# Kernel tuning notes

Measured on AMD Instinct MI355X. Metric: run time of the kernel, lower is better.

Reference implementation:

```python
import jax, jax.numpy as jnp
import numpy as np

NUM_RELATION = 500
NUM_ENTITY = 100000
EMBED_DIM = 64
B, N = 8192, 128
MASK_BIG = 1e19


def setup_inputs() -> dict:
    key = jax.random.key(0)
    k1, k2, k3, k4, k5, k6, k7, k8 = jax.random.split(key, 8)
    inp = {
        "input": jax.random.normal(k1, (B, N, EMBED_DIM), dtype=jnp.float32),
        "neighbor": jax.random.randint(k2, (B, N, 2), 0, NUM_ENTITY + 1, dtype=jnp.int64),
        "query_relation_id": jax.random.randint(k3, (B,), 0, 2 * NUM_RELATION, dtype=jnp.int64),
        "weight": jax.random.uniform(k4, (B, N, 2), dtype=jnp.float32),
        # learned parameters (xavier-normal-like init)
        "mlp_w_weight": jax.random.normal(k5, (NUM_ENTITY * 2 + 1, EMBED_DIM), dtype=jnp.float32) * 0.02,
        "qrel_weight": jax.random.normal(k6, (NUM_RELATION * 2, EMBED_DIM), dtype=jnp.float32) * 0.02,
        "att_w": jax.random.normal(k7, (EMBED_DIM * 2, EMBED_DIM * 2), dtype=jnp.float32) * 0.05,
        "att_v": jax.random.normal(k8, (1, EMBED_DIM * 2), dtype=jnp.float32) * 0.05,
    }
    return inp


def reference(input, neighbor, query_relation_id, weight, mlp_w_weight, qrel_weight, att_w, att_v):
    # neighbor channels: relation id (indexes mlp_w), entity id (indexes mask tables)
    input_relation = neighbor[:, :, 0]
    input_entity = neighbor[:, :, 1]

    r = mlp_w_weight[input_relation]                         # [B,N,D] gather
    # hyperplane transform: e - <e, r_hat> r_hat  (F.normalize with eps=1e-12)
    norm = jnp.maximum(jnp.linalg.norm(r, axis=2, keepdims=True), 1e-12)
    normed = r / norm
    transformed = input - jnp.sum(input * normed, axis=2, keepdims=True) * normed

    # mask_emb: 1 for real entities, 0 for padding entity (id == NUM_ENTITY)
    mask = (input_entity < NUM_ENTITY).astype(transformed.dtype)[:, :, None]
    transformed = transformed * mask

    query = qrel_weight[query_relation_id][:, None, :]       # [B,1,D]
    query = jnp.broadcast_to(query, (query.shape[0], transformed.shape[1], query.shape[2]))

    # MLP attention: tanh([q; t] W) . v
    hidden = jnp.tanh(jnp.concatenate([query, transformed], axis=2) @ att_w)  # [B,N,2D]
    attention_logit = jnp.sum(hidden * att_v[0], axis=2)      # [B,N]

    # mask_weight: subtract 1e19 at padding entities
    mask_logit = jnp.where(input_entity == NUM_ENTITY, jnp.float32(MASK_BIG), jnp.float32(0.0))
    attention_logit = attention_logit - mask_logit

    attention_weight = jax.nn.softmax(attention_logit, axis=1)
    attention_weight = attention_weight + weight[:, :, 0] / (weight[:, :, 1] + 1)

    output = jnp.sum(transformed * attention_weight[:, :, None], axis=1)  # [B,D]
    return output, attention_weight
```

## Files before the change

### kernel.cpp

```cpp
#include <hip/hip_runtime.h>
#include <hip/hip_bf16.h>

#define NB 8192
#define NE 100000

typedef __bf16 bf16x8 __attribute__((ext_vector_type(8)));
typedef __bf16 bf16x4 __attribute__((ext_vector_type(4)));
typedef float  f32x4  __attribute__((ext_vector_type(4)));

template<int C>
__device__ __forceinline__ float dpp_mov(float v) {
  return __int_as_float(__builtin_amdgcn_update_dpp(
      0, __float_as_int(v), C, 0xF, 0xF, true));
}

__device__ __forceinline__ float red16(float v) {
  v += dpp_mov<0xB1>(v);
  v += dpp_mov<0x4E>(v);
  v += dpp_mov<0x141>(v);
  v += dpp_mov<0x140>(v);
  return v;
}

__device__ __forceinline__ float fast_tanh(float x) {
  float e = __expf(-2.0f * fabsf(x));
  float t = (1.0f - e) * __builtin_amdgcn_rcpf(1.0f + e);
  return copysignf(t, x);
}

__global__ void prep_kernel(const float* __restrict__ att_w,
                            const float* __restrict__ qrel,
                            __bf16* __restrict__ wsf,
                            float*  __restrict__ qpart) {
  const int t = threadIdx.x;
  const int bid = blockIdx.x;
  if (bid == 0) {
    for (int i = t; i < 8192; i += 128) {
      int e  = i & 7;
      int l  = (i >> 3) & 63;
      int ks = (i >> 9) & 1;
      int tc = i >> 10;
      int k = ks * 32 + ((l >> 4) << 3) + e;
      int j = tc * 16 + (l & 15);
      wsf[i] = (__bf16)att_w[(64 + k) * 128 + j];
    }
  } else {
    int rid = bid - 1;
    float acc = 0.f;
    for (int k = 0; k < 64; ++k)
      acc += qrel[rid * 64 + k] * att_w[k * 128 + t];
    qpart[rid * 128 + t] = acc;
  }
}

__global__ __launch_bounds__(256, 6)
void attn_kernel(const float* __restrict__ inp,
                 const int*   __restrict__ nb,
                 const int*   __restrict__ qid_p,
                 const float* __restrict__ wgt,
                 const float* __restrict__ mlp,
                 const float* __restrict__ attv,
                 const __bf16* __restrict__ wsf,
                 const float* __restrict__ qpart_t,
                 float* __restrict__ out) {
  __shared__ __attribute__((aligned(16))) __bf16 T16[128][72];
  __shared__ float qp[128], plog[128], awl[128], wrat[128];
  __shared__ float part[4][64];

  const int t    = threadIdx.x;
  const int lane = t & 63;
  const int w    = t >> 6;
  const int g    = lane >> 4;
  const int q    = lane & 15;
  const int b    = blockIdx.x;

  if (t < 128) {
    int qid = qid_p[b];
    qp[t] = qpart_t[qid * 128 + t];
    float2 w01 = reinterpret_cast<const float2*>(wgt)[(size_t)b * 128 + t];
    wrat[t] = w01.x / (w01.y + 1.0f);
  }

  {
    int2 re[8];
#pragma unroll
    for (int i = 0; i < 8; ++i) {
      int n = w * 32 + i * 4 + g;
      re[i] = *reinterpret_cast<const int2*>(&nb[((size_t)b * 128 + n) * 2]);
    }
#pragma unroll
    for (int i = 0; i < 8; ++i) {
      int n = w * 32 + i * 4 + g;
      f32x4 iv = *reinterpret_cast<const f32x4*>(&inp[((size_t)b * 128 + n) * 64 + q * 4]);
      f32x4 rv = *reinterpret_cast<const f32x4*>(&mlp[(size_t)re[i].x * 64 + q * 4]);
      float s1 = red16(rv[0]*rv[0] + rv[1]*rv[1] + rv[2]*rv[2] + rv[3]*rv[3]);
      float s2 = red16(iv[0]*rv[0] + iv[1]*rv[1] + iv[2]*rv[2] + iv[3]*rv[3]);
      float f  = s2 / fmaxf(s1, 1e-24f);
      float m  = (re[i].y >= NE) ? 0.0f : 1.0f;
      bf16x4 tv;
#pragma unroll
      for (int j = 0; j < 4; ++j) tv[j] = (__bf16)((iv[j] - f * rv[j]) * m);
      *reinterpret_cast<bf16x4*>(&T16[n][q * 4]) = tv;
    }
  }
  __syncthreads();

  float vv[8];
#pragma unroll
  for (int tc = 0; tc < 8; ++tc) vv[tc] = attv[tc * 16 + q];

  f32x4 acc[2][8];
#pragma unroll
  for (int tc = 0; tc < 8; ++tc) {
    float qv = qp[tc * 16 + q];
    acc[0][tc] = f32x4{qv, qv, qv, qv};
    acc[1][tc] = f32x4{qv, qv, qv, qv};
  }
  bf16x8 af[2][2];
#pragma unroll
  for (int tr = 0; tr < 2; ++tr) {
    int row = w * 32 + tr * 16 + q;
    af[tr][0] = *reinterpret_cast<const bf16x8*>(&T16[row][g * 8]);
    af[tr][1] = *reinterpret_cast<const bf16x8*>(&T16[row][g * 8 + 32]);
  }
#pragma unroll
  for (int tc = 0; tc < 8; ++tc) {
    bf16x8 b0 = *reinterpret_cast<const bf16x8*>(wsf + ((tc * 2 + 0) * 64 + lane) * 8);
    bf16x8 b1 = *reinterpret_cast<const bf16x8*>(wsf + ((tc * 2 + 1) * 64 + lane) * 8);
    acc[0][tc] = __builtin_amdgcn_mfma_f32_16x16x32_bf16(af[0][0], b0, acc[0][tc], 0, 0, 0);
    acc[1][tc] = __builtin_amdgcn_mfma_f32_16x16x32_bf16(af[1][0], b0, acc[1][tc], 0, 0, 0);
    acc[0][tc] = __builtin_amdgcn_mfma_f32_16x16x32_bf16(af[0][1], b1, acc[0][tc], 0, 0, 0);
    acc[1][tc] = __builtin_amdgcn_mfma_f32_16x16x32_bf16(af[1][1], b1, acc[1][tc], 0, 0, 0);
  }

#pragma unroll
  for (int tr = 0; tr < 2; ++tr) {
    float p0 = 0.f, p1 = 0.f, p2 = 0.f, p3 = 0.f;
#pragma unroll
    for (int tc = 0; tc < 8; ++tc) {
      p0 += fast_tanh(acc[tr][tc][0]) * vv[tc];
      p1 += fast_tanh(acc[tr][tc][1]) * vv[tc];
      p2 += fast_tanh(acc[tr][tc][2]) * vv[tc];
      p3 += fast_tanh(acc[tr][tc][3]) * vv[tc];
    }
    p0 = red16(p0); p1 = red16(p1); p2 = red16(p2); p3 = red16(p3);
    if (q == 0) {
      int row = w * 32 + tr * 16 + g * 4;
      plog[row + 0] = p0;
      plog[row + 1] = p1;
      plog[row + 2] = p2;
      plog[row + 3] = p3;
    }
  }
  __syncthreads();

  if (w == 0) {
    int e0i = nb[((size_t)b * 128 + lane) * 2 + 1];
    int e1i = nb[((size_t)b * 128 + lane + 64) * 2 + 1];
    float l0 = plog[lane]      - ((e0i == NE) ? 1e19f : 0.0f);
    float l1 = plog[lane + 64] - ((e1i == NE) ? 1e19f : 0.0f);
    float m = fmaxf(l0, l1);
    m = fmaxf(m, __shfl_xor(m, 1, 64));
    m = fmaxf(m, __shfl_xor(m, 2, 64));
    m = fmaxf(m, __shfl_xor(m, 4, 64));
    m = fmaxf(m, __shfl_xor(m, 8, 64));
    m = fmaxf(m, __shfl_xor(m, 16, 64));
    m = fmaxf(m, __shfl_xor(m, 32, 64));
    float e0 = __expf(l0 - m), e1 = __expf(l1 - m);
    float s = e0 + e1;
    s += __shfl_xor(s, 1, 64);
    s += __shfl_xor(s, 2, 64);
    s += __shfl_xor(s, 4, 64);
    s += __shfl_xor(s, 8, 64);
    s += __shfl_xor(s, 16, 64);
    s += __shfl_xor(s, 32, 64);
    float inv = 1.0f / s;
    float a0 = e0 * inv + wrat[lane];
    float a1 = e1 * inv + wrat[lane + 64];
    awl[lane] = a0; awl[lane + 64] = a1;
    float* awout = out + (size_t)NB * 64;
    awout[(size_t)b * 128 + lane]      = a0;
    awout[(size_t)b * 128 + lane + 64] = a1;
  }
  __syncthreads();

  {
    float s = 0.f;
#pragma unroll 8
    for (int i = 0; i < 32; ++i) {
      int n = w * 32 + i;
      s += (float)T16[n][lane] * awl[n];
    }
    part[w][lane] = s;
  }
  __syncthreads();
  if (t < 64)
    out[(size_t)b * 64 + t] = part[0][t] + part[1][t] + part[2][t] + part[3][t];
}

extern "C" void kernel_launch(void* const* d_in, const int* in_sizes, int n_in,
                              void* d_out, int out_size, void* d_ws, size_t ws_size,
                              hipStream_t stream) {
  const float* inp  = (const float*)d_in[0];
  const int*   nb   = (const int*)d_in[1];
  const int*   qid  = (const int*)d_in[2];
  const float* wgt  = (const float*)d_in[3];
  const float* mlp  = (const float*)d_in[4];
  const float* qrel = (const float*)d_in[5];
  const float* attw = (const float*)d_in[6];
  const float* attv = (const float*)d_in[7];
  float* out = (float*)d_out;

  __bf16* wsf   = (__bf16*)d_ws;
  float*  qpart = (float*)((char*)d_ws + 16384);

  prep_kernel<<<1001, 128, 0, stream>>>(attw, qrel, wsf, qpart);
  attn_kernel<<<NB, 256, 0, stream>>>(inp, nb, qid, wgt, mlp, attv, wsf, qpart, out);
}
```

Before: 508.5 us.

## Make attention kernel stages wave-local, dropping block barriers and vectorizing reduction

Each wave now writes and reads only its own 32 rows of the transformed tile, mask and attention weights. That lets two of the block-wide __syncthreads be replaced by an LDS waitcnt, and every wave computes the softmax redundantly instead of only wave 0. Query partials, attention vectors and weight ratios are loaded straight into registers. The MFMA/tanh stage is split into two halves so fewer accumulators are live, and launch bounds drop from 6 to 4 waves. The final weighted sum uses vectorized bf16x4 LDS reads with swizzle/shuffle reductions; the risks are lower occupancy and the redundant softmax work in every wave.

```diff
diff --git a/kernel.cpp b/kernel.cpp
--- a/kernel.cpp
+++ b/kernel.cpp
@@ -20,6 +20,10 @@
   v += dpp_mov<0x141>(v);
   v += dpp_mov<0x140>(v);
   return v;
+}
+
+__device__ __forceinline__ float swz_xor16(float v) {
+  return __int_as_float(__builtin_amdgcn_ds_swizzle(__float_as_int(v), 0x401F));
 }
 
 __device__ __forceinline__ float fast_tanh(float x) {
@@ -53,7 +57,7 @@
   }
 }
 
-__global__ __launch_bounds__(256, 6)
+__global__ __launch_bounds__(256, 4)
 void attn_kernel(const float* __restrict__ inp,
                  const int*   __restrict__ nb,
                  const int*   __restrict__ qid_p,
@@ -64,7 +68,7 @@
                  const float* __restrict__ qpart_t,
                  float* __restrict__ out) {
   __shared__ __attribute__((aligned(16))) __bf16 T16[128][72];
-  __shared__ float qp[128], plog[128], awl[128], wrat[128];
+  __shared__ float plog[128], mlog[128], awl[128];
   __shared__ float part[4][64];
 
   const int t    = threadIdx.x;
@@ -74,12 +78,16 @@
   const int q    = lane & 15;
   const int b    = blockIdx.x;
 
-  if (t < 128) {
-    int qid = qid_p[b];
-    qp[t] = qpart_t[qid * 128 + t];
-    float2 w01 = reinterpret_cast<const float2*>(wgt)[(size_t)b * 128 + t];
-    wrat[t] = w01.x / (w01.y + 1.0f);
-  }
+  const int qid = qid_p[b];
+  float qpv[8], vv[8];
+#pragma unroll
+  for (int tc = 0; tc < 8; ++tc) {
+    qpv[tc] = qpart_t[qid * 128 + tc * 16 + q];
+    vv[tc]  = attv[tc * 16 + q];
+  }
+  const int rown = w * 32 + (lane & 31);
+  float2 w01 = reinterpret_cast<const float2*>(wgt)[(size_t)b * 128 + rown];
+  const float wr = w01.x / (w01.y + 1.0f);
 
   {
     int2 re[8];
@@ -101,21 +109,11 @@
 #pragma unroll
       for (int j = 0; j < 4; ++j) tv[j] = (__bf16)((iv[j] - f * rv[j]) * m);
       *reinterpret_cast<bf16x4*>(&T16[n][q * 4]) = tv;
-    }
-  }
-  __syncthreads();
-
-  float vv[8];
-#pragma unroll
-  for (int tc = 0; tc < 8; ++tc) vv[tc] = attv[tc * 16 + q];
-
-  f32x4 acc[2][8];
-#pragma unroll
-  for (int tc = 0; tc < 8; ++tc) {
-    float qv = qp[tc * 16 + q];
-    acc[0][tc] = f32x4{qv, qv, qv, qv};
-    acc[1][tc] = f32x4{qv, qv, qv, qv};
-  }
+      if (q == 0) mlog[n] = (re[i].y == NE) ? 1e19f : 0.0f;
+    }
+  }
+  asm volatile("s_waitcnt lgkmcnt(0)" ::: "memory");
+
   bf16x8 af[2][2];
 #pragma unroll
   for (int tr = 0; tr < 2; ++tr) {
@@ -123,27 +121,41 @@
     af[tr][0] = *reinterpret_cast<const bf16x8*>(&T16[row][g * 8]);
     af[tr][1] = *reinterpret_cast<const bf16x8*>(&T16[row][g * 8 + 32]);
   }
-#pragma unroll
-  for (int tc = 0; tc < 8; ++tc) {
-    bf16x8 b0 = *reinterpret_cast<const bf16x8*>(wsf + ((tc * 2 + 0) * 64 + lane) * 8);
-    bf16x8 b1 = *reinterpret_cast<const bf16x8*>(wsf + ((tc * 2 + 1) * 64 + lane) * 8);
-    acc[0][tc] = __builtin_amdgcn_mfma_f32_16x16x32_bf16(af[0][0], b0, acc[0][tc], 0, 0, 0);
-    acc[1][tc] = __builtin_amdgcn_mfma_f32_16x16x32_bf16(af[1][0], b0, acc[1][tc], 0, 0, 0);
-    acc[0][tc] = __builtin_amdgcn_mfma_f32_16x16x32_bf16(af[0][1], b1, acc[0][tc], 0, 0, 0);
-    acc[1][tc] = __builtin_amdgcn_mfma_f32_16x16x32_bf16(af[1][1], b1, acc[1][tc], 0, 0, 0);
-  }
-
+  float p[2][4] = {{0,0,0,0},{0,0,0,0}};
+#pragma unroll
+  for (int h = 0; h < 2; ++h) {
+    f32x4 acc[2][4];
+#pragma unroll
+    for (int tc2 = 0; tc2 < 4; ++tc2) {
+      float qv = qpv[h * 4 + tc2];
+      acc[0][tc2] = f32x4{qv, qv, qv, qv};
+      acc[1][tc2] = f32x4{qv, qv, qv, qv};
+    }
+#pragma unroll
+    for (int tc2 = 0; tc2 < 4; ++tc2) {
+      int tc = h * 4 + tc2;
+      bf16x8 b0 = *reinterpret_cast<const bf16x8*>(wsf + ((tc * 2 + 0) * 64 + lane) * 8);
+      bf16x8 b1 = *reinterpret_cast<const bf16x8*>(wsf + ((tc * 2 + 1) * 64 + lane) * 8);
+      acc[0][tc2] = __builtin_amdgcn_mfma_f32_16x16x32_bf16(af[0][0], b0, acc[0][tc2], 0, 0, 0);
+      acc[1][tc2] = __builtin_amdgcn_mfma_f32_16x16x32_bf16(af[1][0], b0, acc[1][tc2], 0, 0, 0);
+      acc[0][tc2] = __builtin_amdgcn_mfma_f32_16x16x32_bf16(af[0][1], b1, acc[0][tc2], 0, 0, 0);
+      acc[1][tc2] = __builtin_amdgcn_mfma_f32_16x16x32_bf16(af[1][1], b1, acc[1][tc2], 0, 0, 0);
+    }
+#pragma unroll
+    for (int tr = 0; tr < 2; ++tr)
+#pragma unroll
+      for (int tc2 = 0; tc2 < 4; ++tc2) {
+        float v = vv[h * 4 + tc2];
+        p[tr][0] += fast_tanh(acc[tr][tc2][0]) * v;
+        p[tr][1] += fast_tanh(acc[tr][tc2][1]) * v;
+        p[tr][2] += fast_tanh(acc[tr][tc2][2]) * v;
+        p[tr][3] += fast_tanh(acc[tr][tc2][3]) * v;
+      }
+  }
 #pragma unroll
   for (int tr = 0; tr < 2; ++tr) {
-    float p0 = 0.f, p1 = 0.f, p2 = 0.f, p3 = 0.f;
-#pragma unroll
-    for (int tc = 0; tc < 8; ++tc) {
-      p0 += fast_tanh(acc[tr][tc][0]) * vv[tc];
-      p1 += fast_tanh(acc[tr][tc][1]) * vv[tc];
-      p2 += fast_tanh(acc[tr][tc][2]) * vv[tc];
-      p3 += fast_tanh(acc[tr][tc][3]) * vv[tc];
-    }
-    p0 = red16(p0); p1 = red16(p1); p2 = red16(p2); p3 = red16(p3);
+    float p0 = red16(p[tr][0]), p1 = red16(p[tr][1]);
+    float p2 = red16(p[tr][2]), p3 = red16(p[tr][3]);
     if (q == 0) {
       int row = w * 32 + tr * 16 + g * 4;
       plog[row + 0] = p0;
@@ -154,11 +166,9 @@
   }
   __syncthreads();
 
-  if (w == 0) {
-    int e0i = nb[((size_t)b * 128 + lane) * 2 + 1];
-    int e1i = nb[((size_t)b * 128 + lane + 64) * 2 + 1];
-    float l0 = plog[lane]      - ((e0i == NE) ? 1e19f : 0.0f);
-    float l1 = plog[lane + 64] - ((e1i == NE) ? 1e19f : 0.0f);
+  {
+    float l0 = plog[lane]      - mlog[lane];
+    float l1 = plog[lane + 64] - mlog[lane + 64];
     float m = fmaxf(l0, l1);
     m = fmaxf(m, __shfl_xor(m, 1, 64));
     m = fmaxf(m, __shfl_xor(m, 2, 64));
@@ -174,24 +184,37 @@
     s += __shfl_xor(s, 8, 64);
     s += __shfl_xor(s, 16, 64);
     s += __shfl_xor(s, 32, 64);
-    float inv = 1.0f / s;
-    float a0 = e0 * inv + wrat[lane];
-    float a1 = e1 * inv + wrat[lane + 64];
-    awl[lane] = a0; awl[lane + 64] = a1;
-    float* awout = out + (size_t)NB * 64;
-    awout[(size_t)b * 128 + lane]      = a0;
-    awout[(size_t)b * 128 + lane + 64] = a1;
-  }
-  __syncthreads();
+    float inv = __builtin_amdgcn_rcpf(s) * (2.0f - s * __builtin_amdgcn_rcpf(s));
+    float lg = plog[rown] - mlog[rown];
+    float aw = __expf(lg - m) * inv + wr;
+    if (lane < 32) {
+      awl[rown] = aw;
+      float* awout = out + (size_t)NB * 64;
+      awout[(size_t)b * 128 + rown] = aw;
+    }
+  }
+  asm volatile("s_waitcnt lgkmcnt(0)" ::: "memory");
 
   {
-    float s = 0.f;
-#pragma unroll 8
-    for (int i = 0; i < 32; ++i) {
-      int n = w * 32 + i;
-      s += (float)T16[n][lane] * awl[n];
-    }
-    part[w][lane] = s;
+    f32x4 s4 = {0.f, 0.f, 0.f, 0.f};
+#pragma unroll
+    for (int i = 0; i < 8; ++i) {
+      int n = w * 32 + i * 4 + g;
+      bf16x4 tv = *reinterpret_cast<const bf16x4*>(&T16[n][q * 4]);
+      float a = awl[n];
+      s4[0] += (float)tv[0] * a;
+      s4[1] += (float)tv[1] * a;
+      s4[2] += (float)tv[2] * a;
+      s4[3] += (float)tv[3] * a;
+    }
+#pragma unroll
+    for (int c = 0; c < 4; ++c) {
+      float v = s4[c];
+      v += swz_xor16(v);
+      v += __shfl_xor(v, 32, 64);
+      s4[c] = v;
+    }
+    if (lane < 16) *reinterpret_cast<f32x4*>(&part[w][lane * 4]) = s4;
   }
   __syncthreads();
   if (t < 64)
```

Result: faster. 475.7 us (-6.4%).
